# Optimization experiments

Hardware: AMD Instinct MI355X
Metric: run time of the kernel (lower is better)

Reference implementation:

```python
import jax, jax.numpy as jnp
import numpy as np

N_ENTITY = 200000
N_RELATIONS = 32
DIM = 64
N_HOP = 2
N_MEMORY = 32
BATCH = 1024
KGE_WEIGHT = 0.01
L2_WEIGHT = 1e-7


def setup_inputs() -> dict:
    key = jax.random.key(0)
    ks = jax.random.split(key, 8)
    items = jax.random.randint(ks[0], (BATCH,), 0, N_ENTITY)
    labels = jax.random.uniform(ks[1], (BATCH,), dtype=jnp.float32)
    memories_h = jax.random.randint(ks[2], (N_HOP, BATCH, N_MEMORY), 0, N_ENTITY)
    memories_r = jax.random.randint(ks[3], (N_HOP, BATCH, N_MEMORY), 0, N_RELATIONS)
    memories_t = jax.random.randint(ks[4], (N_HOP, BATCH, N_MEMORY), 0, N_ENTITY)
    item_table = jax.random.normal(ks[5], (N_ENTITY, DIM), dtype=jnp.float32) * 0.1
    relation_table = jax.random.normal(ks[6], (N_RELATIONS, DIM * DIM), dtype=jnp.float32) * 0.1
    transform_W = jax.random.normal(ks[7], (DIM, DIM), dtype=jnp.float32) * 0.1
    return dict(items=items, labels=labels, memories_h=memories_h,
                memories_r=memories_r, memories_t=memories_t,
                item_table=item_table, relation_table=relation_table,
                transform_W=transform_W)


def _forward(items, labels, memories_h, memories_r, memories_t,
             item_table, relation_table, transform_W):
    v = item_table[items]  # [B, D]
    o_list = []
    kge_loss = jnp.float32(0.0)
    l2_loss = jnp.float32(0.0)
    for hop in range(N_HOP):
        h = item_table[memories_h[hop]]                                   # [B, M, D]
        R = relation_table[memories_r[hop]].reshape(-1, N_MEMORY, DIM, DIM)  # [B, M, D, D]
        t = item_table[memories_t[hop]]                                   # [B, M, D]
        # Rh = R @ h  -> [B, M, D]
        Rh = jnp.einsum('bmij,bmj->bmi', R, h)
        # attention probs over memory slots
        probs = jax.nn.softmax(jnp.einsum('bmi,bi->bm', Rh, v), axis=-1)  # [B, M]
        o = jnp.einsum('bmd,bm->bd', t, probs)                            # [B, D]
        # item_update_mode == 'plus_transform': v = W(v + o)
        v = (v + o) @ transform_W.T
        o_list.append(o)
        # KGE loss: sigmoid(h^T R t), mean over [B, M]
        hRt = jnp.einsum('bmi,bmij,bmj->bm', h, R, t)
        kge_loss = kge_loss + jnp.mean(jax.nn.sigmoid(hRt))
        l2_loss = l2_loss + jnp.sum(h * h) + jnp.sum(t * t) + jnp.sum(R * R)
    kge_loss = -KGE_WEIGHT * kge_loss
    l2_loss = L2_WEIGHT * l2_loss
    # predict with all hops
    y = o_list[-1]
    for i in range(N_HOP - 1):
        y = y + o_list[i]
    scores = jax.nn.sigmoid(jnp.sum(v * y, axis=1))  # [B]
    # BCE loss (torch clamps log at -100)
    logp = jnp.clip(jnp.log(scores), -100.0)
    lognp = jnp.clip(jnp.log(1.0 - scores), -100.0)
    base_loss = -jnp.mean(labels * logp + (1.0 - labels) * lognp)
    loss = base_loss + kge_loss + l2_loss
    return scores, loss, base_loss, kge_loss, l2_loss


def reference(items, labels, memories_h, memories_r, memories_t,
              item_table, relation_table, transform_W):
    return _forward(items, labels, memories_h, memories_r, memories_t,
                    item_table, relation_table, transform_W)
```

## Files before the change

### kernel.cpp

```cpp
#include <hip/hip_runtime.h>
#include <math.h>

#define N_ENTITY 200000
#define N_REL 32
#define DIM 64
#define N_HOP 2
#define N_MEM 32
#define BATCH 1024
#define PAIR_PER_HOP (BATCH * N_MEM)
#define N_PAIR (N_HOP * PAIR_PER_HOP)
#define CAP 3072
#define JBLK 32
#define WPB 4
#define NBLK_PAIRS (JBLK * N_REL * WPB)
#define TPAD 68

typedef __attribute__((ext_vector_type(8))) short short8;
typedef __attribute__((ext_vector_type(4))) float floatx4;

__device__ __forceinline__ float wave_reduce_sum(float v) {
    v += __shfl_xor(v, 1);
    v += __shfl_xor(v, 2);
    v += __shfl_xor(v, 4);
    v += __shfl_xor(v, 8);
    v += __shfl_xor(v, 16);
    v += __shfl_xor(v, 32);
    return v;
}

__device__ __forceinline__ unsigned short f2b(float x) {
    union { float f; unsigned u; } c; c.f = x;
    const unsigned r = (c.u + 0x7FFFu + ((c.u >> 16) & 1u)) >> 16;
    return (unsigned short)r;
}

__device__ __forceinline__ short8 pack8(const float4 a, const float4 b) {
    short8 s;
    s[0] = (short)f2b(a.x); s[1] = (short)f2b(a.y);
    s[2] = (short)f2b(a.z); s[3] = (short)f2b(a.w);
    s[4] = (short)f2b(b.x); s[5] = (short)f2b(b.y);
    s[6] = (short)f2b(b.z); s[7] = (short)f2b(b.w);
    return s;
}

__device__ __forceinline__ float sq4(const float4 a) {
    return a.x * a.x + a.y * a.y + a.z * a.z + a.w * a.w;
}

__device__ __forceinline__ float dot4(const float4 a, const float4 b) {
    return a.x * b.x + a.y * b.y + a.z * b.z + a.w * b.w;
}

__global__ __launch_bounds__(256) void ripple_bin(
    const int* __restrict__ mr,
    int* __restrict__ g_cnt,
    int* __restrict__ list)
{
    __shared__ int hist[N_REL];
    __shared__ int cur[N_REL];
    const int tid = (int)threadIdx.x;
    const int pbase = (int)blockIdx.x * 1024;

    if (tid < N_REL) hist[tid] = 0;
    __syncthreads();

    int rv[4];
    #pragma unroll
    for (int u = 0; u < 4; ++u) {
        rv[u] = mr[pbase + u * 256 + tid];
        atomicAdd(&hist[rv[u]], 1);
    }
    __syncthreads();
    if (tid < N_REL) cur[tid] = atomicAdd(&g_cnt[tid], hist[tid]);
    __syncthreads();
    #pragma unroll
    for (int u = 0; u < 4; ++u) {
        const int r = rv[u];
        const int pos = atomicAdd(&cur[r], 1);
        if (pos < CAP) list[r * CAP + pos] = pbase + u * 256 + tid;
    }
}

__global__ __launch_bounds__(256) void ripple_pairs(
    const int* __restrict__ items,
    const int* __restrict__ mh,
    const int* __restrict__ mt,
    const float* __restrict__ item_table,
    const float* __restrict__ rel_table,
    const int* __restrict__ g_cnt,
    const int* __restrict__ list,
    float* __restrict__ wsL,
    float* __restrict__ wsRh,
    float* __restrict__ ws_kge,
    float* __restrict__ ws_l2)
{
    __shared__ __align__(16) float sTr[WPB][2][16 * TPAD];

    const int tid = (int)threadIdx.x;
    const int lane = tid & 63;
    const int w = tid >> 6;
    const int j = (int)blockIdx.x;
    const int r = (int)blockIdx.y;
    const int n = min(g_cnt[r], CAP);

    const int m16 = lane & 15;
    const int quad = lane >> 4;
    const int rb = r * CAP;
    const int wave_id = j * WPB + w;

    float* __restrict__ bufC = &sTr[w][0][0];
    float* __restrict__ bufT = &sTr[w][1][0];

    int tau = wave_id;
    int p = 0, hidx = 0, tidx = 0;
    if (tau * 16 < n) {
        const int pos = min(tau * 16 + m16, n - 1);
        p = list[rb + pos];
        hidx = mh[p];
        tidx = mt[p];
    }

    short8 Bf[2][4];
    float rsq = 0.f;
    {
        const float* __restrict__ Rb = rel_table + (size_t)r * (DIM * DIM);
        #pragma unroll
        for (int s = 0; s < 2; ++s) {
            #pragma unroll
            for (int tn = 0; tn < 4; ++tn) {
                const float* src = Rb + (size_t)(16 * tn + m16) * DIM + 32 * s + 8 * quad;
                const float4 a = *(const float4*)src;
                const float4 b = *(const float4*)(src + 4);
                rsq += sq4(a) + sq4(b);
                Bf[s][tn] = pack8(a, b);
            }
        }
    }

    float kge = 0.f;
    float l2ht = 0.f;
    int cnt = 0;

    for (; tau * 16 < n; tau += JBLK * WPB) {
        const int base = tau * 16;
        const bool mvalid = (base + m16) < n;

        const float* __restrict__ hp = item_table + (size_t)hidx * DIM + 8 * quad;
        const float* __restrict__ tp = item_table + (size_t)tidx * DIM + 8 * quad;
        const float4 h0a = *(const float4*)hp;
        const float4 h0b = *(const float4*)(hp + 4);
        const float4 h1a = *(const float4*)(hp + 32);
        const float4 h1b = *(const float4*)(hp + 36);
        const float4 t0a = *(const float4*)tp;
        const float4 t0b = *(const float4*)(tp + 4);
        const float4 t1a = *(const float4*)(tp + 32);
        const float4 t1b = *(const float4*)(tp + 36);

        const int tau2 = tau + JBLK * WPB;
        int p2 = 0, h2 = 0, t2 = 0;
        if (tau2 * 16 < n) {
            const int pos2 = min(tau2 * 16 + m16, n - 1);
            p2 = list[rb + pos2];
            h2 = mh[p2];
            t2 = mt[p2];
        }

        if (mvalid) {
            l2ht += sq4(h0a) + sq4(h0b) + sq4(h1a) + sq4(h1b)
                  + sq4(t0a) + sq4(t0b) + sq4(t1a) + sq4(t1b);
        }

        const short8 Ah0 = pack8(h0a, h0b);
        const short8 Ah1 = pack8(h1a, h1b);
        const short8 At0 = pack8(t0a, t0b);
        const short8 At1 = pack8(t1a, t1b);

        floatx4 Ch[4], Ct[4];
        const floatx4 z4 = {0.f, 0.f, 0.f, 0.f};
        #pragma unroll
        for (int tn = 0; tn < 4; ++tn) {
            Ch[tn] = __builtin_amdgcn_mfma_f32_16x16x32_bf16(Ah0, Bf[0][tn], z4, 0, 0, 0);
            Ch[tn] = __builtin_amdgcn_mfma_f32_16x16x32_bf16(Ah1, Bf[1][tn], Ch[tn], 0, 0, 0);
            Ct[tn] = __builtin_amdgcn_mfma_f32_16x16x32_bf16(At0, Bf[0][tn], z4, 0, 0, 0);
            Ct[tn] = __builtin_amdgcn_mfma_f32_16x16x32_bf16(At1, Bf[1][tn], Ct[tn], 0, 0, 0);
        }

        #pragma unroll
        for (int tn = 0; tn < 4; ++tn) {
            const int col = m16 + 16 * tn;
            #pragma unroll
            for (int q = 0; q < 4; ++q) {
                const int row = 4 * quad + q;
                bufC[row * TPAD + col] = Ch[tn][q];
                bufT[row * TPAD + col] = Ct[tn][q];
            }
        }

        const float* rowT = bufT + m16 * TPAD;
        const float4 ct0 = *(const float4*)(rowT + 8 * quad);
        const float4 ct1 = *(const float4*)(rowT + 8 * quad + 4);
        const float4 ct2 = *(const float4*)(rowT + 32 + 8 * quad);
        const float4 ct3 = *(const float4*)(rowT + 32 + 8 * quad + 4);
        float hrt = dot4(h0a, ct0) + dot4(h0b, ct1) + dot4(h1a, ct2) + dot4(h1b, ct3);
        hrt += __shfl_xor(hrt, 16);
        hrt += __shfl_xor(hrt, 32);

        const float* rowC = bufC + m16 * TPAD;
        const float4 c0 = *(const float4*)(rowC + 16 * quad);
        const float4 c1 = *(const float4*)(rowC + 16 * quad + 4);
        const float4 c2 = *(const float4*)(rowC + 16 * quad + 8);
        const float4 c3 = *(const float4*)(rowC + 16 * quad + 12);

        const bool hop0 = p < PAIR_PER_HOP;
        float lg = 0.f;
        if (hop0) {
            const float* __restrict__ vp =
                item_table + (size_t)items[p >> 5] * DIM + 16 * quad;
            lg = dot4(*(const float4*)vp, c0)
               + dot4(*(const float4*)(vp + 4), c1)
               + dot4(*(const float4*)(vp + 8), c2)
               + dot4(*(const float4*)(vp + 12), c3);
        }
        lg += __shfl_xor(lg, 16);
        lg += __shfl_xor(lg, 32);

        if (quad == 0 && mvalid) {
            kge += 1.f / (1.f + expf(-hrt));
            if (hop0) wsL[p] = lg;
        }

        if (mvalid && !hop0) {
            float* __restrict__ dst =
                wsRh + (size_t)(p - PAIR_PER_HOP) * DIM + 16 * quad;
            *(float4*)dst = c0;
            *(float4*)(dst + 4) = c1;
            *(float4*)(dst + 8) = c2;
            *(float4*)(dst + 12) = c3;
        }

        cnt += min(16, n - base);
        p = p2; hidx = h2; tidx = t2;
    }

    const float Rsum = wave_reduce_sum(rsq);
    const float l2tot = wave_reduce_sum(l2ht) + (float)cnt * Rsum;
    const float kgetot = wave_reduce_sum(kge);
    if (lane == 0) {
        const int bid = (r * JBLK + j) * WPB + w;
        ws_kge[bid] = kgetot;
        ws_l2[bid] = l2tot;
    }
}

__global__ __launch_bounds__(256) void ripple_attn(
    const int* __restrict__ items,
    const float* __restrict__ labels,
    const int* __restrict__ mt,
    const float* __restrict__ item_table,
    const float* __restrict__ W,
    const float* __restrict__ wsL,
    const float* __restrict__ wsRh,
    float* __restrict__ out,
    float* __restrict__ ws_bce)
{
    __shared__ float sAtt[N_MEM];
    __shared__ __align__(16) float sO[4][DIM];
    __shared__ __align__(16) float sU[DIM];
    __shared__ __align__(16) float sV[DIM];

    const int b = (int)blockIdx.x;
    const int tid = (int)threadIdx.x;
    const int lane = tid & 63;
    const int w = tid >> 6;

    float v_i = item_table[(size_t)items[b] * DIM + lane];
    float y_i = 0.f;

    for (int hop = 0; hop < N_HOP; ++hop) {
        if (hop == 0) {
            if (tid < N_MEM) sAtt[tid] = wsL[b * N_MEM + tid];
        } else {
            const int m = tid >> 3;
            const int d0 = (tid & 7) * 8;
            const float* __restrict__ rp =
                wsRh + (size_t)(b * N_MEM + m) * DIM + d0;
            const float4 ra = *(const float4*)rp;
            const float4 rb4 = *(const float4*)(rp + 4);
            const float4 va = *(const float4*)&sV[d0];
            const float4 vb = *(const float4*)&sV[d0 + 4];
            float dp = ra.x * va.x + ra.y * va.y + ra.z * va.z + ra.w * va.w
                     + rb4.x * vb.x + rb4.y * vb.y + rb4.z * vb.z + rb4.w * vb.w;
            dp += __shfl_xor(dp, 1);
            dp += __shfl_xor(dp, 2);
            dp += __shfl_xor(dp, 4);
            if ((tid & 7) == 0) sAtt[m] = dp;
        }
        __syncthreads();

        float mx = -1e30f;
        #pragma unroll
        for (int m = 0; m < N_MEM; ++m) mx = fmaxf(mx, sAtt[m]);
        float se = 0.f;
        float e_loc[8];
        #pragma unroll
        for (int m = 0; m < N_MEM; ++m) {
            const float e = expf(sAtt[m] - mx);
            se += e;
            if ((m >> 3) == w) e_loc[m & 7] = e;
        }
        const float inv = 1.f / se;

        float op = 0.f;
        #pragma unroll
        for (int q = 0; q < 8; ++q) {
            const int m = w * 8 + q;
            const int tidx = mt[hop * PAIR_PER_HOP + b * N_MEM + m];
            op = fmaf(item_table[(size_t)tidx * DIM + lane], e_loc[q] * inv, op);
        }
        sO[w][lane] = op;
        __syncthreads();

        const float o_i = sO[0][lane] + sO[1][lane] + sO[2][lane] + sO[3][lane];
        y_i += o_i;
        if (w == 0) sU[lane] = v_i + o_i;
        __syncthreads();

        const float4* __restrict__ Wrow = (const float4*)(W + (size_t)lane * DIM);
        float a0 = 0.f, a1 = 0.f, a2 = 0.f, a3 = 0.f;
        #pragma unroll
        for (int k = 0; k < 16; ++k) {
            const float4 w4 = Wrow[k];
            const float4 u4 = *(const float4*)&sU[k * 4];
            a0 = fmaf(w4.x, u4.x, a0);
            a1 = fmaf(w4.y, u4.y, a1);
            a2 = fmaf(w4.z, u4.z, a2);
            a3 = fmaf(w4.w, u4.w, a3);
        }
        v_i = (a0 + a1) + (a2 + a3);
        if (w == 0) sV[lane] = v_i;
        __syncthreads();
    }

    float s = wave_reduce_sum(v_i * y_i);
    s = 1.f / (1.f + expf(-s));
    if (tid == 0) {
        out[b] = s;
        const float lab = labels[b];
        const float logp = fmaxf(logf(s), -100.f);
        const float lognp = fmaxf(logf(1.f - s), -100.f);
        ws_bce[b] = lab * logp + (1.f - lab) * lognp;
    }
}

__global__ __launch_bounds__(256) void ripple_finalize(
    const float* __restrict__ ws_bce,
    const float* __restrict__ ws_kge,
    const float* __restrict__ ws_l2,
    float* __restrict__ out)
{
    __shared__ float sb[4], sk[4], sl[4];
    const int tid = (int)threadIdx.x;
    float bsum = 0.f, ksum = 0.f, lsum = 0.f;
    for (int i = tid; i < BATCH; i += 256) bsum += ws_bce[i];
    for (int i = tid; i < NBLK_PAIRS; i += 256) {
        ksum += ws_kge[i];
        lsum += ws_l2[i];
    }
    bsum = wave_reduce_sum(bsum);
    ksum = wave_reduce_sum(ksum);
    lsum = wave_reduce_sum(lsum);
    const int w = tid >> 6;
    if ((tid & 63) == 0) { sb[w] = bsum; sk[w] = ksum; sl[w] = lsum; }
    __syncthreads();
    if (tid == 0) {
        const float bs = sb[0] + sb[1] + sb[2] + sb[3];
        const float ks = sk[0] + sk[1] + sk[2] + sk[3];
        const float ls = sl[0] + sl[1] + sl[2] + sl[3];
        const float base_loss = -bs / (float)BATCH;
        const float kge_loss = -0.01f * (ks / (float)(BATCH * N_MEM));
        const float l2_loss = 1e-7f * ls;
        out[BATCH + 0] = base_loss + kge_loss + l2_loss;
        out[BATCH + 1] = base_loss;
        out[BATCH + 2] = kge_loss;
        out[BATCH + 3] = l2_loss;
    }
}

extern "C" void kernel_launch(void* const* d_in, const int* in_sizes, int n_in,
                              void* d_out, int out_size, void* d_ws, size_t ws_size,
                              hipStream_t stream) {
    const int* items        = (const int*)d_in[0];
    const float* labels     = (const float*)d_in[1];
    const int* mh           = (const int*)d_in[2];
    const int* mr           = (const int*)d_in[3];
    const int* mt           = (const int*)d_in[4];
    const float* item_table = (const float*)d_in[5];
    const float* rel_table  = (const float*)d_in[6];
    const float* W          = (const float*)d_in[7];
    float* out = (float*)d_out;

    float* ws = (float*)d_ws;
    float* wsL    = ws;
    float* wsRh   = wsL + PAIR_PER_HOP;
    int*   list   = (int*)(wsRh + (size_t)PAIR_PER_HOP * DIM);
    int*   g_cnt  = list + N_REL * CAP;
    float* ws_bce = (float*)(g_cnt + N_REL);
    float* ws_kge = ws_bce + BATCH;
    float* ws_l2  = ws_kge + NBLK_PAIRS;

    hipMemsetAsync(g_cnt, 0, N_REL * sizeof(int), stream);
    ripple_bin<<<N_PAIR / 1024, 256, 0, stream>>>(mr, g_cnt, list);
    dim3 gpairs(JBLK, N_REL);
    ripple_pairs<<<gpairs, 256, 0, stream>>>(items, mh, mt, item_table, rel_table,
                                             g_cnt, list, wsL, wsRh, ws_kge, ws_l2);
    ripple_attn<<<BATCH, 256, 0, stream>>>(items, labels, mt, item_table, W,
                                           wsL, wsRh, out, ws_bce);
    ripple_finalize<<<1, 256, 0, stream>>>(ws_bce, ws_kge, ws_l2, out);
}
```

Baseline: 144.6 us.

## Fuse finalize into attention via last-block counter, share R fragments through LDS

The finalize kernel is folded into ripple_attn. Each block bumps a global done counter after a threadfence, and the last block to finish performs the loss reduction, which removes one kernel launch. In ripple_pairs the relation-matrix fragments are now loaded once per block into LDS, cooperatively and with the squared-sum reduced across waves, instead of every wave loading the full matrix. The per-wave transpose buffer is also halved by reusing one buffer for the T and H results in turn, which lowers LDS footprint and could raise occupancy.

Result: slower. 161.7 us (+11.8%).

```diff
diff --git a/kernel.cpp b/kernel.cpp
--- a/kernel.cpp
+++ b/kernel.cpp
@@ -94,7 +94,9 @@
     float* __restrict__ ws_kge,
     float* __restrict__ ws_l2)
 {
-    __shared__ __align__(16) float sTr[WPB][2][16 * TPAD];
+    __shared__ __align__(16) float sTr[WPB][16 * TPAD];
+    __shared__ __align__(16) short8 sB[512];
+    __shared__ float sRed[WPB];
 
     const int tid = (int)threadIdx.x;
     const int lane = tid & 63;
@@ -108,8 +110,7 @@
     const int rb = r * CAP;
     const int wave_id = j * WPB + w;
 
-    float* __restrict__ bufC = &sTr[w][0][0];
-    float* __restrict__ bufT = &sTr[w][1][0];
+    float* __restrict__ buf = &sTr[w][0];
 
     int tau = wave_id;
     int p = 0, hidx = 0, tidx = 0;
@@ -120,22 +121,34 @@
         tidx = mt[p];
     }
 
-    short8 Bf[2][4];
-    float rsq = 0.f;
     {
         const float* __restrict__ Rb = rel_table + (size_t)r * (DIM * DIM);
-        #pragma unroll
-        for (int s = 0; s < 2; ++s) {
-            #pragma unroll
-            for (int tn = 0; tn < 4; ++tn) {
-                const float* src = Rb + (size_t)(16 * tn + m16) * DIM + 32 * s + 8 * quad;
-                const float4 a = *(const float4*)src;
-                const float4 b = *(const float4*)(src + 4);
-                rsq += sq4(a) + sq4(b);
-                Bf[s][tn] = pack8(a, b);
-            }
-        }
-    }
+        float rsq = 0.f;
+        #pragma unroll
+        for (int u = 0; u < 2; ++u) {
+            const int slot = tid + 256 * u;
+            const int s = slot >> 8;
+            const int tn = (slot >> 6) & 3;
+            const int ls = slot & 63;
+            const float* src = Rb + (size_t)(16 * tn + (ls & 15)) * DIM
+                             + 32 * s + 8 * (ls >> 4);
+            const float4 a = *(const float4*)src;
+            const float4 b = *(const float4*)(src + 4);
+            rsq += sq4(a) + sq4(b);
+            sB[slot] = pack8(a, b);
+        }
+        rsq = wave_reduce_sum(rsq);
+        if (lane == 0) sRed[w] = rsq;
+    }
+    __syncthreads();
+    const float Rsum = sRed[0] + sRed[1] + sRed[2] + sRed[3];
+
+    short8 Bf[2][4];
+    #pragma unroll
+    for (int s = 0; s < 2; ++s)
+        #pragma unroll
+        for (int tn = 0; tn < 4; ++tn)
+            Bf[s][tn] = sB[s * 256 + tn * 64 + lane];
 
     float kge = 0.f;
     float l2ht = 0.f;
@@ -189,14 +202,10 @@
         for (int tn = 0; tn < 4; ++tn) {
             const int col = m16 + 16 * tn;
             #pragma unroll
-            for (int q = 0; q < 4; ++q) {
-                const int row = 4 * quad + q;
-                bufC[row * TPAD + col] = Ch[tn][q];
-                bufT[row * TPAD + col] = Ct[tn][q];
-            }
-        }
-
-        const float* rowT = bufT + m16 * TPAD;
+            for (int q = 0; q < 4; ++q)
+                buf[(4 * quad + q) * TPAD + col] = Ct[tn][q];
+        }
+        const float* rowT = buf + m16 * TPAD;
         const float4 ct0 = *(const float4*)(rowT + 8 * quad);
         const float4 ct1 = *(const float4*)(rowT + 8 * quad + 4);
         const float4 ct2 = *(const float4*)(rowT + 32 + 8 * quad);
@@ -205,7 +214,14 @@
         hrt += __shfl_xor(hrt, 16);
         hrt += __shfl_xor(hrt, 32);
 
-        const float* rowC = bufC + m16 * TPAD;
+        #pragma unroll
+        for (int tn = 0; tn < 4; ++tn) {
+            const int col = m16 + 16 * tn;
+            #pragma unroll
+            for (int q = 0; q < 4; ++q)
+                buf[(4 * quad + q) * TPAD + col] = Ch[tn][q];
+        }
+        const float* rowC = buf + m16 * TPAD;
         const float4 c0 = *(const float4*)(rowC + 16 * quad);
         const float4 c1 = *(const float4*)(rowC + 16 * quad + 4);
         const float4 c2 = *(const float4*)(rowC + 16 * quad + 8);
@@ -242,7 +258,6 @@
         p = p2; hidx = h2; tidx = t2;
     }
 
-    const float Rsum = wave_reduce_sum(rsq);
     const float l2tot = wave_reduce_sum(l2ht) + (float)cnt * Rsum;
     const float kgetot = wave_reduce_sum(kge);
     if (lane == 0) {
@@ -260,13 +275,18 @@
     const float* __restrict__ W,
     const float* __restrict__ wsL,
     const float* __restrict__ wsRh,
-    float* __restrict__ out,
-    float* __restrict__ ws_bce)
+    const float* __restrict__ ws_kge,
+    const float* __restrict__ ws_l2,
+    float* __restrict__ ws_bce,
+    int* __restrict__ done_cnt,
+    float* __restrict__ out)
 {
     __shared__ float sAtt[N_MEM];
     __shared__ __align__(16) float sO[4][DIM];
     __shared__ __align__(16) float sU[DIM];
     __shared__ __align__(16) float sV[DIM];
+    __shared__ int sLast;
+    __shared__ float sb[4], sk[4], sl[4];
 
     const int b = (int)blockIdx.x;
     const int tid = (int)threadIdx.x;
@@ -349,17 +369,13 @@
         const float logp = fmaxf(logf(s), -100.f);
         const float lognp = fmaxf(logf(1.f - s), -100.f);
         ws_bce[b] = lab * logp + (1.f - lab) * lognp;
-    }
-}
-
-__global__ __launch_bounds__(256) void ripple_finalize(
-    const float* __restrict__ ws_bce,
-    const float* __restrict__ ws_kge,
-    const float* __restrict__ ws_l2,
-    float* __restrict__ out)
-{
-    __shared__ float sb[4], sk[4], sl[4];
-    const int tid = (int)threadIdx.x;
+        __threadfence();
+        const int old = atomicAdd(done_cnt, 1);
+        sLast = (old == BATCH - 1) ? 1 : 0;
+    }
+    __syncthreads();
+    if (sLast == 0) return;
+
     float bsum = 0.f, ksum = 0.f, lsum = 0.f;
     for (int i = tid; i < BATCH; i += 256) bsum += ws_bce[i];
     for (int i = tid; i < NBLK_PAIRS; i += 256) {
@@ -369,8 +385,7 @@
     bsum = wave_reduce_sum(bsum);
     ksum = wave_reduce_sum(ksum);
     lsum = wave_reduce_sum(lsum);
-    const int w = tid >> 6;
-    if ((tid & 63) == 0) { sb[w] = bsum; sk[w] = ksum; sl[w] = lsum; }
+    if (lane == 0) { sb[w] = bsum; sk[w] = ksum; sl[w] = lsum; }
     __syncthreads();
     if (tid == 0) {
         const float bs = sb[0] + sb[1] + sb[2] + sb[3];
@@ -404,16 +419,17 @@
     float* wsRh   = wsL + PAIR_PER_HOP;
     int*   list   = (int*)(wsRh + (size_t)PAIR_PER_HOP * DIM);
     int*   g_cnt  = list + N_REL * CAP;
-    float* ws_bce = (float*)(g_cnt + N_REL);
+    int*   done   = g_cnt + N_REL;
+    float* ws_bce = (float*)(done + 1);
     float* ws_kge = ws_bce + BATCH;
     float* ws_l2  = ws_kge + NBLK_PAIRS;
 
-    hipMemsetAsync(g_cnt, 0, N_REL * sizeof(int), stream);
+    hipMemsetAsync(g_cnt, 0, (N_REL + 1) * sizeof(int), stream);
     ripple_bin<<<N_PAIR / 1024, 256, 0, stream>>>(mr, g_cnt, list);
     dim3 gpairs(JBLK, N_REL);
     ripple_pairs<<<gpairs, 256, 0, stream>>>(items, mh, mt, item_table, rel_table,
                                              g_cnt, list, wsL, wsRh, ws_kge, ws_l2);
     ripple_attn<<<BATCH, 256, 0, stream>>>(items, labels, mt, item_table, W,
-                                           wsL, wsRh, out, ws_bce);
-    ripple_finalize<<<1, 256, 0, stream>>>(ws_bce, ws_kge, ws_l2, out);
-}
+                                           wsL, wsRh, ws_kge, ws_l2,
+                                           ws_bce, done, out);
+}
```
